# Kernel tuning notes

Hardware: AMD Instinct MI355X
Metric: run time of the kernel (lower is better)

The kernel has to match this reference:

```python
import jax, jax.numpy as jnp
import numpy as np

DIM, NHEADS = 1024, 16
HD = DIM // NHEADS
ROPE_BASE = 10000.0


def rope_cos_sin(seq_len, hd):
    inv_freq = 1.0 / (ROPE_BASE ** (jnp.arange(0, hd, 2, dtype=jnp.float32) / hd))
    t = jnp.arange(seq_len, dtype=jnp.float32)
    freqs = jnp.outer(t, inv_freq)              # [N, hd/2]
    emb = jnp.concatenate([freqs, freqs], -1)   # [N, hd]
    return jnp.cos(emb), jnp.sin(emb)


def rotate_half(x):
    h = x.shape[-1] // 2
    return jnp.concatenate([-x[..., h:], x[..., :h]], -1)


def setup_inputs() -> dict:
    key = jax.random.key(0)
    ks = jax.random.split(key, 5)
    B, N = 1, 2048
    x = jax.random.normal(ks[0], (B, N, DIM), jnp.float32)
    wq = jax.random.normal(ks[1], (DIM, DIM), jnp.float32) * 0.02
    wk = jax.random.normal(ks[2], (DIM, DIM), jnp.float32) * 0.02
    wv = jax.random.normal(ks[3], (DIM, DIM), jnp.float32) * 0.02
    wp = jax.random.normal(ks[4], (DIM, DIM), jnp.float32) * 0.02
    return {"x": x, "wq": wq, "wk": wk, "wv": wv, "wp": wp}


def reference(x, wq, wk, wv, wp):
    B, N, D = x.shape
    H, hd = NHEADS, HD
    # nn.Linear: y = x @ W.T (weights stored [out, in])
    q = (x @ wq.T).reshape(B, N, H, hd)
    k = (x @ wk.T).reshape(B, N, H, hd)
    v = (x @ wv.T).reshape(B, N, H, hd)
    cos, sin = rope_cos_sin(N, hd)
    cos = cos[None, :, None, :]
    sin = sin[None, :, None, :]
    q = q * cos + rotate_half(q) * sin
    k = k * cos + rotate_half(k) * sin
    # SDPA (no mask, non-causal, eval -> no dropout)
    scale = 1.0 / jnp.sqrt(jnp.float32(hd))
    logits = jnp.einsum("bqhd,bkhd->bhqk", q, k) * scale
    attn = jax.nn.softmax(logits, axis=-1)
    out = jnp.einsum("bhqk,bkhd->bqhd", attn, v).reshape(B, N, D)
    return out @ wp.T
```

## Files before the change

kernel.cpp:

```cpp
#include <hip/hip_runtime.h>

typedef short s16x8 __attribute__((ext_vector_type(8)));
typedef float f32x4 __attribute__((ext_vector_type(4)));
typedef float f32x16 __attribute__((ext_vector_type(16)));

__device__ __forceinline__ unsigned short f2bf(float f) {
    unsigned int u = __float_as_uint(f);
    u += 0x7fff + ((u >> 16) & 1);
    return (unsigned short)(u >> 16);
}
__device__ __forceinline__ float bf2f(unsigned short h) {
    return __uint_as_float(((unsigned int)h) << 16);
}
__device__ __forceinline__ f32x4 mfma16(s16x8 a, s16x8 b, f32x4 c) {
    return __builtin_amdgcn_mfma_f32_16x16x32_bf16(a, b, c, 0, 0, 0);
}
__device__ __forceinline__ f32x16 mfma32(s16x8 a, s16x8 b, f32x16 c) {
    return __builtin_amdgcn_mfma_f32_32x32x16_bf16(a, b, c, 0, 0, 0);
}
__device__ __forceinline__ void async16(const void* g, void* l) {
    __builtin_amdgcn_global_load_lds(
        (const __attribute__((address_space(1))) void*)g,
        (__attribute__((address_space(3))) void*)l, 16, 0, 0);
}

__global__ __launch_bounds__(256) void convert_all(
    const float* __restrict__ x,  const float* __restrict__ wq,
    const float* __restrict__ wk, const float* __restrict__ wv,
    const float* __restrict__ wp,
    unsigned short* __restrict__ xb, unsigned short* __restrict__ wqkvb,
    unsigned short* __restrict__ wpb)
{
    const size_t XN = 2048u * 1024u, WN = 1024u * 1024u;
    size_t e = ((size_t)blockIdx.x * 256 + threadIdx.x) * 4;
    const float* s; unsigned short* d;
    if (e < XN)                { s = x  + e;               d = xb    + e; }
    else if (e < XN + WN)      { s = wq + (e - XN);        d = wqkvb + (e - XN); }
    else if (e < XN + 2 * WN)  { s = wk + (e - XN - WN);   d = wqkvb + (e - XN); }
    else if (e < XN + 3 * WN)  { s = wv + (e - XN - 2*WN); d = wqkvb + (e - XN); }
    else                       { s = wp + (e - XN - 3*WN); d = wpb   + (e - XN - 3*WN); }
    float4 v = *(const float4*)s;
    ushort4 o;
    o.x = f2bf(v.x); o.y = f2bf(v.y); o.z = f2bf(v.z); o.w = f2bf(v.w);
    *(ushort4*)d = o;
}

template<int BM, int BN, int C32>
__global__ __launch_bounds__(256) void gemm_mfma(
    const unsigned short* __restrict__ A,
    const unsigned short* __restrict__ B,
    void* __restrict__ C, int Ntot)
{
    constexpr int MT = BM / 32, NT = BN / 32;
    __shared__ unsigned short As[BM * 128];
    __shared__ unsigned short Bs[BN * 128];

    const int tid  = threadIdx.x;
    const int wave = tid >> 6, lane = tid & 63;
    const int l16  = lane & 15, quad = lane >> 4;
    const int m0   = blockIdx.y * BM, n0 = blockIdx.x * BN;
    const int wm   = (wave & 1) * (BM / 2), wn = (wave >> 1) * (BN / 2);

    const int r4 = lane >> 4;
    const int c8 = (lane & 15) * 8;

    f32x4 acc[MT][NT] = {};

    for (int k0 = 0; k0 < 1024; k0 += 128) {
        #pragma unroll
        for (int i = 0; i < BM / 16; i++) {
            int rg = wave * (BM / 16) + i;
            async16(A + (size_t)(m0 + rg * 4 + r4) * 1024 + k0 + c8, &As[rg * 512]);
        }
        #pragma unroll
        for (int i = 0; i < BN / 16; i++) {
            int rg = wave * (BN / 16) + i;
            async16(B + (size_t)(n0 + rg * 4 + r4) * 1024 + k0 + c8, &Bs[rg * 512]);
        }
        __syncthreads();

        #pragma unroll
        for (int ks = 0; ks < 4; ks++) {
            s16x8 af[MT], bfr[NT];
            #pragma unroll
            for (int mt = 0; mt < MT; mt++)
                af[mt] = *(const s16x8*)&As[(wm + mt * 16 + l16) * 128 + ks * 32 + quad * 8];
            #pragma unroll
            for (int nt = 0; nt < NT; nt++)
                bfr[nt] = *(const s16x8*)&Bs[(wn + nt * 16 + l16) * 128 + ks * 32 + quad * 8];
            #pragma unroll
            for (int mt = 0; mt < MT; mt++)
                #pragma unroll
                for (int nt = 0; nt < NT; nt++)
                    acc[mt][nt] = mfma16(af[mt], bfr[nt], acc[mt][nt]);
        }
        __syncthreads();
    }

    #pragma unroll
    for (int mt = 0; mt < MT; mt++)
        #pragma unroll
        for (int nt = 0; nt < NT; nt++)
            #pragma unroll
            for (int r = 0; r < 4; r++) {
                int m = m0 + wm + mt * 16 + quad * 4 + r;
                int n = n0 + wn + nt * 16 + l16;
                size_t idx = (size_t)m * Ntot + n;
                if (C32) ((float*)C)[idx] = acc[mt][nt][r];
                else     ((unsigned short*)C)[idx] = f2bf(acc[mt][nt][r]);
            }
}

__global__ __launch_bounds__(256) void rope_kernel(unsigned short* __restrict__ qkv)
{
    int idx = blockIdx.x * 256 + threadIdx.x;
    int i = idx & 31;
    int h = (idx >> 5) & 15;
    int n = idx >> 9;
    float ang = (float)n * exp2f((float)i * (-13.287712379549449f / 32.0f));
    float c, s;
    sincosf(ang, &c, &s);
    size_t base = (size_t)n * 3072 + h * 64 + i;
    float a0 = bf2f(qkv[base]), a1 = bf2f(qkv[base + 32]);
    qkv[base]      = f2bf(a0 * c + a1 * s);
    qkv[base + 32] = f2bf(a1 * c - a0 * s);
    float b0 = bf2f(qkv[base + 1024]), b1 = bf2f(qkv[base + 1056]);
    qkv[base + 1024] = f2bf(b0 * c + b1 * s);
    qkv[base + 1056] = f2bf(b1 * c - b0 * s);
}

__global__ __launch_bounds__(256, 4) void attn_part(
    const unsigned short* __restrict__ qkv,
    float* __restrict__ Opart, float* __restrict__ Lpart)
{
    const int h  = blockIdx.y;
    const int q0 = blockIdx.x * 128;
    const int ks = blockIdx.z;
    const int tid  = threadIdx.x;
    const int wave = tid >> 6, lane = tid & 63;
    const int l32  = lane & 31, half = lane >> 5;

    __shared__ unsigned short Ks[64][72];
    __shared__ unsigned short Vt[64][72];
    __shared__ unsigned short Ps[4][32][72];

    const unsigned short* qp = qkv + (size_t)(q0 + wave * 32 + l32) * 3072 + h * 64 + half * 8;
    s16x8 qb[4];
    #pragma unroll
    for (int c = 0; c < 4; c++)
        qb[c] = *(const s16x8*)(qp + c * 16);

    f32x16 o0 = {}, o1 = {};
    float lsum = 0.f;

    for (int t = 0; t < 8; t++) {
        const int kt = ks * 512 + t * 64;

        if (tid < 128) {
            int g  = tid & 15;
            int d0 = (tid >> 4) * 8;
            const unsigned short* gv = qkv + (size_t)(kt + 4 * g) * 3072 + 2048 + h * 64 + d0;
            unsigned short a0[8], a1[8], a2[8], a3[8];
            *(uint4*)a0 = *(const uint4*)gv;
            *(uint4*)a1 = *(const uint4*)(gv + 3072);
            *(uint4*)a2 = *(const uint4*)(gv + 6144);
            *(uint4*)a3 = *(const uint4*)(gv + 9216);
            #pragma unroll
            for (int d = 0; d < 8; d++) {
                ushort4 w;
                w.x = a0[d]; w.y = a1[d]; w.z = a2[d]; w.w = a3[d];
                *(ushort4*)&Vt[d0 + d][4 * g] = w;
            }
        } else {
            int u = tid - 128;
            int key = u & 63;
            int dh = (u >> 6) * 32;
            const unsigned short* gk = qkv + (size_t)(kt + key) * 3072 + 1024 + h * 64 + dh;
            const uint4* g4 = (const uint4*)gk;
            uint4 k0 = g4[0], k1 = g4[1], k2 = g4[2], k3 = g4[3];
            *(uint4*)&Ks[key][dh]      = k0;
            *(uint4*)&Ks[key][dh + 8]  = k1;
            *(uint4*)&Ks[key][dh + 16] = k2;
            *(uint4*)&Ks[key][dh + 24] = k3;
        }
        __syncthreads();

        #pragma unroll
        for (int g = 0; g < 2; g++) {
            f32x16 s = {};
            #pragma unroll
            for (int c = 0; c < 4; c++) {
                s16x8 ka = *(const s16x8*)&Ks[g * 32 + l32][c * 16 + half * 8];
                s = mfma32(ka, qb[c], s);
            }
            #pragma unroll
            for (int c = 0; c < 4; c++) {
                float e0 = __expf(s[4 * c + 0] * 0.125f);
                float e1 = __expf(s[4 * c + 1] * 0.125f);
                float e2 = __expf(s[4 * c + 2] * 0.125f);
                float e3 = __expf(s[4 * c + 3] * 0.125f);
                lsum += (e0 + e1) + (e2 + e3);
                ushort4 w;
                w.x = f2bf(e0); w.y = f2bf(e1); w.z = f2bf(e2); w.w = f2bf(e3);
                *(ushort4*)&Ps[wave][l32][g * 32 + c * 8 + half * 4] = w;
            }
        }

        #pragma unroll
        for (int c = 0; c < 4; c++) {
            s16x8 pa = *(const s16x8*)&Ps[wave][l32][c * 16 + half * 8];
            s16x8 v0 = *(const s16x8*)&Vt[l32][c * 16 + half * 8];
            s16x8 v1 = *(const s16x8*)&Vt[32 + l32][c * 16 + half * 8];
            o0 = mfma32(pa, v0, o0);
            o1 = mfma32(pa, v1, o1);
        }
        __syncthreads();
    }

    lsum += __shfl_xor(lsum, 32, 64);

    const int mq = q0 + wave * 32;
    float* opBase = Opart + (size_t)ks * 2048 * 1024;
    #pragma unroll
    for (int r = 0; r < 16; r++) {
        int qr = (r & 3) + 8 * (r >> 2) + 4 * half;
        float* op = opBase + (size_t)(mq + qr) * 1024 + h * 64;
        op[l32]      = o0[r];
        op[32 + l32] = o1[r];
    }
    if (half == 0)
        Lpart[((size_t)ks * 2048 + mq + l32) * 16 + h] = lsum;
}

__global__ __launch_bounds__(256) void combine(
    const float* __restrict__ Opart, const float* __restrict__ Lpart,
    unsigned short* __restrict__ ab)
{
    size_t e = ((size_t)blockIdx.x * 256 + threadIdx.x) * 4;
    int tok = (int)(e >> 10);
    int h = (int)((e & 1023) >> 6);
    float l = 0.f;
    #pragma unroll
    for (int s = 0; s < 4; s++)
        l += Lpart[((size_t)s * 2048 + tok) * 16 + h];
    float inv = 1.0f / l;
    float4 acc = *(const float4*)(Opart + e);
    #pragma unroll
    for (int s = 1; s < 4; s++) {
        float4 n = *(const float4*)(Opart + (size_t)s * 2048 * 1024 + e);
        acc.x += n.x; acc.y += n.y; acc.z += n.z; acc.w += n.w;
    }
    ushort4 w;
    w.x = f2bf(acc.x * inv);
    w.y = f2bf(acc.y * inv);
    w.z = f2bf(acc.z * inv);
    w.w = f2bf(acc.w * inv);
    *(ushort4*)(ab + e) = w;
}

extern "C" void kernel_launch(void* const* d_in, const int* in_sizes, int n_in,
                              void* d_out, int out_size, void* d_ws, size_t ws_size,
                              hipStream_t stream)
{
    const float* x  = (const float*)d_in[0];
    const float* wq = (const float*)d_in[1];
    const float* wk = (const float*)d_in[2];
    const float* wv = (const float*)d_in[3];
    const float* wp = (const float*)d_in[4];

    unsigned short* xb    = (unsigned short*)d_ws;
    unsigned short* wqkvb = xb    + 2u * 1024 * 1024;
    unsigned short* wpb   = wqkvb + 3u * 1024 * 1024;
    unsigned short* qkv   = wpb   + 1u * 1024 * 1024;
    unsigned short* ab    = qkv   + 2048u * 3072;
    float* Opart = (float*)(ab + 2u * 1024 * 1024);
    float* Lpart = Opart + 4u * 2048 * 1024;

    convert_all<<<6144, 256, 0, stream>>>(x, wq, wk, wv, wp, xb, wqkvb, wpb);
    gemm_mfma<128, 64, 0><<<dim3(48, 16), 256, 0, stream>>>(xb, wqkvb, qkv, 3072);
    rope_kernel<<<(2048 * 512) / 256, 256, 0, stream>>>(qkv);
    attn_part<<<dim3(16, 16, 4), 256, 0, stream>>>(qkv, Opart, Lpart);
    combine<<<2048, 256, 0, stream>>>(Opart, Lpart, ab);
    gemm_mfma<64, 64, 1><<<dim3(16, 32), 256, 0, stream>>>(ab, wpb, d_out, 1024);
}
```

Baseline: 177.5 us.

## Enlarge QKV GEMM tiles, halve K-step, split-K output projection with reduction

The GEMM kernel now stages 64-wide K slices in shared memory instead of 128, which halves LDS use, and takes a K-range per blockIdx.z. The QKV projection uses 128x128 tiles (24x16 grid) for more reuse per block. The output projection is split across two K halves that write fp32 partials, followed by a small reduction kernel. This trades an extra launch and extra partial-buffer traffic for more blocks in flight on the small output GEMM.

After: 163.1 us. 8.1% less time.

```diff
diff --git a/kernel.cpp b/kernel.cpp
--- a/kernel.cpp
+++ b/kernel.cpp
@@ -49,45 +49,46 @@
 __global__ __launch_bounds__(256) void gemm_mfma(
     const unsigned short* __restrict__ A,
     const unsigned short* __restrict__ B,
-    void* __restrict__ C, int Ntot)
+    void* __restrict__ C, int Ntot, int kLen, size_t cSlice)
 {
     constexpr int MT = BM / 32, NT = BN / 32;
-    __shared__ unsigned short As[BM * 128];
-    __shared__ unsigned short Bs[BN * 128];
+    __shared__ unsigned short As[BM * 64];
+    __shared__ unsigned short Bs[BN * 64];
 
     const int tid  = threadIdx.x;
     const int wave = tid >> 6, lane = tid & 63;
     const int l16  = lane & 15, quad = lane >> 4;
     const int m0   = blockIdx.y * BM, n0 = blockIdx.x * BN;
+    const int kB   = blockIdx.z * kLen;
     const int wm   = (wave & 1) * (BM / 2), wn = (wave >> 1) * (BN / 2);
 
-    const int r4 = lane >> 4;
-    const int c8 = (lane & 15) * 8;
+    const int srow8 = lane >> 3;
+    const int scol  = (lane & 7) * 8;
 
     f32x4 acc[MT][NT] = {};
 
-    for (int k0 = 0; k0 < 1024; k0 += 128) {
-        #pragma unroll
-        for (int i = 0; i < BM / 16; i++) {
-            int rg = wave * (BM / 16) + i;
-            async16(A + (size_t)(m0 + rg * 4 + r4) * 1024 + k0 + c8, &As[rg * 512]);
-        }
-        #pragma unroll
-        for (int i = 0; i < BN / 16; i++) {
-            int rg = wave * (BN / 16) + i;
-            async16(B + (size_t)(n0 + rg * 4 + r4) * 1024 + k0 + c8, &Bs[rg * 512]);
+    for (int k0 = kB; k0 < kB + kLen; k0 += 64) {
+        #pragma unroll
+        for (int i = 0; i < BM / 32; i++) {
+            int j = wave * (BM / 32) + i;
+            async16(A + (size_t)(m0 + j * 8 + srow8) * 1024 + k0 + scol, &As[j * 512]);
+        }
+        #pragma unroll
+        for (int i = 0; i < BN / 32; i++) {
+            int j = wave * (BN / 32) + i;
+            async16(B + (size_t)(n0 + j * 8 + srow8) * 1024 + k0 + scol, &Bs[j * 512]);
         }
         __syncthreads();
 
         #pragma unroll
-        for (int ks = 0; ks < 4; ks++) {
+        for (int ks = 0; ks < 2; ks++) {
             s16x8 af[MT], bfr[NT];
             #pragma unroll
             for (int mt = 0; mt < MT; mt++)
-                af[mt] = *(const s16x8*)&As[(wm + mt * 16 + l16) * 128 + ks * 32 + quad * 8];
+                af[mt] = *(const s16x8*)&As[(wm + mt * 16 + l16) * 64 + ks * 32 + quad * 8];
             #pragma unroll
             for (int nt = 0; nt < NT; nt++)
-                bfr[nt] = *(const s16x8*)&Bs[(wn + nt * 16 + l16) * 128 + ks * 32 + quad * 8];
+                bfr[nt] = *(const s16x8*)&Bs[(wn + nt * 16 + l16) * 64 + ks * 32 + quad * 8];
             #pragma unroll
             for (int mt = 0; mt < MT; mt++)
                 #pragma unroll
@@ -105,10 +106,21 @@
             for (int r = 0; r < 4; r++) {
                 int m = m0 + wm + mt * 16 + quad * 4 + r;
                 int n = n0 + wn + nt * 16 + l16;
-                size_t idx = (size_t)m * Ntot + n;
+                size_t idx = (size_t)blockIdx.z * cSlice + (size_t)m * Ntot + n;
                 if (C32) ((float*)C)[idx] = acc[mt][nt][r];
                 else     ((unsigned short*)C)[idx] = f2bf(acc[mt][nt][r]);
             }
+}
+
+__global__ __launch_bounds__(256) void reduce_proj(
+    const float* __restrict__ P, float* __restrict__ out)
+{
+    size_t e = ((size_t)blockIdx.x * 256 + threadIdx.x) * 4;
+    float4 a = *(const float4*)(P + e);
+    float4 b = *(const float4*)(P + (size_t)2048 * 1024 + e);
+    float4 o;
+    o.x = a.x + b.x; o.y = a.y + b.y; o.z = a.z + b.z; o.w = a.w + b.w;
+    *(float4*)(out + e) = o;
 }
 
 __global__ __launch_bounds__(256) void rope_kernel(unsigned short* __restrict__ qkv)
@@ -273,13 +285,17 @@
     unsigned short* wpb   = wqkvb + 3u * 1024 * 1024;
     unsigned short* qkv   = wpb   + 1u * 1024 * 1024;
     unsigned short* ab    = qkv   + 2048u * 3072;
-    float* Opart = (float*)(ab + 2u * 1024 * 1024);
-    float* Lpart = Opart + 4u * 2048 * 1024;
+    float* Opart    = (float*)(ab + 2u * 1024 * 1024);
+    float* Lpart    = Opart + 4u * 2048 * 1024;
+    float* projPart = Lpart + 4u * 2048 * 16;
 
     convert_all<<<6144, 256, 0, stream>>>(x, wq, wk, wv, wp, xb, wqkvb, wpb);
-    gemm_mfma<128, 64, 0><<<dim3(48, 16), 256, 0, stream>>>(xb, wqkvb, qkv, 3072);
+    gemm_mfma<128, 128, 0><<<dim3(24, 16, 1), 256, 0, stream>>>(
+        xb, wqkvb, qkv, 3072, 1024, 0);
     rope_kernel<<<(2048 * 512) / 256, 256, 0, stream>>>(qkv);
     attn_part<<<dim3(16, 16, 4), 256, 0, stream>>>(qkv, Opart, Lpart);
     combine<<<2048, 256, 0, stream>>>(Opart, Lpart, ab);
-    gemm_mfma<64, 64, 1><<<dim3(16, 32), 256, 0, stream>>>(ab, wpb, d_out, 1024);
-}
+    gemm_mfma<64, 64, 1><<<dim3(16, 32, 2), 256, 0, stream>>>(
+        ab, wpb, projPart, 1024, 512, (size_t)2048 * 1024);
+    reduce_proj<<<2048, 256, 0, stream>>>(projPart, (float*)d_out);
+}
```
